# Optimization experiments

Hardware: AMD Instinct MI355X
Metric: run time of the kernel (lower is better)

Reference implementation:

```python
import jax, jax.numpy as jnp
import numpy as np

WINDOW_SIZE = 11
SIGMA = 1.5
C1 = (0.01 * 1.0) ** 2
C2 = (0.03 * 1.0) ** 2


def _gauss1d(k, sigma):
    x = np.arange(k, dtype=np.float64) - k // 2
    g = np.exp(-(x ** 2) / (2.0 * sigma ** 2)) / (np.sqrt(2.0 * np.pi) * sigma)
    return (g / g.sum()).astype(np.float32)


def _blur3d(x, g):
    # Separable 3D Gaussian blur, SAME padding. Math-equal to the full 11^3
    # kernel conv in the torch code since the 3D window is an outer product
    # of the normalized 1D Gaussian (symmetric, so conv == cross-corr).
    k = g.shape[0]
    p = k // 2
    dn = ('NCDHW', 'OIDHW', 'NCDHW')
    for axis in range(3):
        shape = [1, 1, 1, 1, 1]
        shape[2 + axis] = k
        w = jnp.asarray(g).reshape(shape)
        pad = [(0, 0), (0, 0), (0, 0)]
        pad[axis] = (p, p)
        x = jax.lax.conv_general_dilated(x, w, (1, 1, 1), pad, dimension_numbers=dn)
    return x


def setup_inputs() -> dict:
    key = jax.random.key(0)
    k1, k2 = jax.random.split(key)
    shape = (4, 1, 192, 192, 192)
    gt = jax.random.uniform(k1, shape, dtype=jnp.float32)
    pred = jax.random.uniform(k2, shape, dtype=jnp.float32)
    return {"gt": gt, "pred": pred}


def reference(gt, pred):
    g = _gauss1d(WINDOW_SIZE, SIGMA)
    mux = _blur3d(gt, g)
    muy = _blur3d(pred, g)
    mux_sq = mux * mux
    muy_sq = muy * muy
    mux_muy = mux * muy
    sigmax_sq = _blur3d(gt * gt, g) - mux_sq
    sigmay_sq = _blur3d(pred * pred, g) - muy_sq
    sigmaxy = _blur3d(gt * pred, g) - mux_muy
    ssim_map = ((2.0 * mux_muy + C1) * (2.0 * sigmaxy + C2)) / (
        (mux_sq + muy_sq + C1) * (sigmax_sq + sigmay_sq + C2))
    return jnp.mean(1.0 - ssim_map)
```

## Files before the change

### kernel.cpp

```cpp
#include <hip/hip_runtime.h>
#include <hip/hip_fp16.h>
#include <math.h>

namespace {
constexpr int S = 192;
constexpr long long S2 = (long long)S * S;
constexpr long long S3 = (long long)S * S2;
constexpr int NB = 4;
constexpr int K = 11;
constexpr int R = 5;
constexpr int HCH = 32;
constexpr int DCH = 48;
constexpr float C1f = 1e-4f;
constexpr float C2f = 9e-4f;

struct GaussW { float g[K]; };

__global__ void k_init(double* acc) { *acc = 0.0; }

__global__ void k_final(const double* __restrict__ acc, float* __restrict__ out) {
  out[0] = (float)(acc[0] / (double)(NB * S3));
}


template <int NROWS, bool GUARD>
__device__ __forceinline__ void stageA(const float* pg, const float* pp, int r0,
                                       int w, float2 (*rb)[208]) {
  float la[NROWS], lb[NROWS];
#pragma unroll
  for (int j = 0; j < NROWS; ++j) {
    int r = r0 + j;
    bool ok = !GUARD || ((unsigned)r < (unsigned)S);
    la[j] = ok ? pg[(long long)r * S + w] : 0.f;
    lb[j] = ok ? pp[(long long)r * S + w] : 0.f;
  }
#pragma unroll
  for (int j = 0; j < NROWS; ++j) rb[j][8 + w] = make_float2(la[j], lb[j]);
}

template <int NROWS, bool EMITALL>
__device__ __forceinline__ void consumeA(
    const float2 (*rb)[208], int w, const GaussW& Wt,
    float2 (&w01)[K], float2 (&w23)[K], float (&w4v)[K],
    uint2* p0123, __half* p4, long long obase, int hbase) {
#pragma unroll
  for (int j = 0; j < NROWS; ++j) {
    float2 s01 = make_float2(0.f, 0.f), s23 = make_float2(0.f, 0.f);
    float s4 = 0.f;
#pragma unroll
    for (int i = 0; i < K; ++i) {
      float2 ab = rb[j][w + 3 + i];
      float g = Wt.g[i];
      s01.x = fmaf(g, ab.x, s01.x);
      s01.y = fmaf(g, ab.y, s01.y);
      float ta = g * ab.x, tb = g * ab.y;
      s23.x = fmaf(ta, ab.x, s23.x);
      s23.y = fmaf(tb, ab.y, s23.y);
      s4 = fmaf(ta, ab.y, s4);
    }
    w01[j] = s01; w23[j] = s23; w4v[j] = s4;
    if (EMITALL || j == K - 1) {
      float2 m01 = make_float2(0.f, 0.f), m23 = make_float2(0.f, 0.f);
      float m4 = 0.f;
#pragma unroll
      for (int i = 0; i < K; ++i) {
        const int sl = (j + 1 + i) % K;
        float g = Wt.g[i];
        m01.x = fmaf(g, w01[sl].x, m01.x);
        m01.y = fmaf(g, w01[sl].y, m01.y);
        m23.x = fmaf(g, w23[sl].x, m23.x);
        m23.y = fmaf(g, w23[sl].y, m23.y);
        m4 = fmaf(g, w4v[sl], m4);
      }
      long long o = obase + (long long)(hbase + j) * S;
      __half2 h01 = __floats2half2_rn(m01.x, m01.y);
      __half2 h23 = __floats2half2_rn(m23.x, m23.y);
      uint2 v;
      v.x = __builtin_bit_cast(unsigned, h01);
      v.y = __builtin_bit_cast(unsigned, h23);
      p0123[o] = v;
      p4[o] = __float2half(m4);
    }
  }
}

__global__ __launch_bounds__(192) void k_blurWH(
    const float* __restrict__ gt, const float* __restrict__ pr,
    uint2* __restrict__ p0123, __half* __restrict__ p4,
    long long in_base, GaussW Wt) {
  __shared__ float2 rowbuf[K][208];
  const int w = threadIdx.x;
  const int dz = blockIdx.x;
  const int h0 = (int)blockIdx.y * HCH;
  const long long n = blockIdx.z;
  const float* pg = gt + in_base + (n * S + dz) * S2;
  const float* pp = pr + in_base + (n * S + dz) * S2;
  const long long obase = (n * S + dz) * S2 + w;

  if (w < 176) {
    int j = w >> 4, q = w & 15;
    rowbuf[j][(q < 8) ? q : (192 + q)] = make_float2(0.f, 0.f);
  }

  float2 w01[K], w23[K];
  float w4v[K];

  stageA<K, true>(pg, pp, h0 - R, w, rowbuf);
  __syncthreads();
  consumeA<K, false>(rowbuf, w, Wt, w01, w23, w4v, p0123, p4, obase, h0 - 10);
  __syncthreads();
  stageA<K, false>(pg, pp, h0 + 6, w, rowbuf);
  __syncthreads();
  consumeA<K, true>(rowbuf, w, Wt, w01, w23, w4v, p0123, p4, obase, h0 + 1);
  __syncthreads();
  stageA<K, false>(pg, pp, h0 + 17, w, rowbuf);
  __syncthreads();
  consumeA<K, true>(rowbuf, w, Wt, w01, w23, w4v, p0123, p4, obase, h0 + 12);
  __syncthreads();
  stageA<9, true>(pg, pp, h0 + 28, w, rowbuf);
  __syncthreads();
  consumeA<9, true>(rowbuf, w, Wt, w01, w23, w4v, p0123, p4, obase, h0 + 23);
}


template <int N, bool GUARD>
__device__ __forceinline__ void stageB(const uint2* q0123, const __half* q4,
                                       int plane0, uint2 (&sab)[K], __half (&se)[K]) {
#pragma unroll
  for (int j = 0; j < N; ++j) {
    int d = plane0 + j;
    bool ok = !GUARD || ((unsigned)d < (unsigned)S);
    long long o = (long long)d * S2;
    sab[j] = ok ? q0123[o] : make_uint2(0u, 0u);
    se[j] = ok ? q4[o] : __float2half(0.f);
  }
}

template <int NOUT>
__device__ __forceinline__ void consumeB(
    const uint2 (&sab)[K], const __half (&se)[K],
    const GaussW& Wt, float2 (&r01)[K], float2 (&r23)[K], float (&r4)[K],
    double& lsum) {
  float fsum = 0.f;
#pragma unroll
  for (int j = 0; j < NOUT; ++j) {
    const int sw = (10 + j) % K;
    r01[sw] = __half22float2(__builtin_bit_cast(__half2, sab[j].x));
    r23[sw] = __half22float2(__builtin_bit_cast(__half2, sab[j].y));
    r4[sw] = __half2float(se[j]);
    float2 m01 = make_float2(0.f, 0.f), m23 = make_float2(0.f, 0.f);
    float m4 = 0.f;
#pragma unroll
    for (int i = 0; i < K; ++i) {
      const int sl = (j + i) % K;
      float g = Wt.g[i];
      m01.x = fmaf(g, r01[sl].x, m01.x);
      m01.y = fmaf(g, r01[sl].y, m01.y);
      m23.x = fmaf(g, r23[sl].x, m23.x);
      m23.y = fmaf(g, r23[sl].y, m23.y);
      m4 = fmaf(g, r4[sl], m4);
    }
    float mux = m01.x, muy = m01.y, bxx = m23.x, byy = m23.y, bxy = m4;
    float mux2 = mux * mux, muy2 = muy * muy, muxy = mux * muy;
    float sx = bxx - mux2, sy = byy - muy2, sxy = bxy - muxy;
    float num = fmaf(2.f, muxy, C1f) * fmaf(2.f, sxy, C2f);
    float den = (mux2 + muy2 + C1f) * (sx + sy + C2f);
    fsum += 1.f - num * __builtin_amdgcn_rcpf(den);
  }
  lsum += (double)fsum;
}

__global__ __launch_bounds__(192) void k_blurD_ssim(
    const uint2* __restrict__ p0123, const __half* __restrict__ p4,
    double* __restrict__ acc, GaussW Wt) {
  const int w = threadIdx.x;
  const int h = blockIdx.x;
  const long long n = blockIdx.y;
  const int d0 = (int)blockIdx.z * DCH;
  const long long base = n * S3 + (long long)h * S + w;
  const uint2* q0123 = p0123 + base;
  const __half* q4 = p4 + base;

  float2 r01[K], r23[K];
  float r4[K];
#pragma unroll
  for (int c = 0; c < K - 1; ++c) {
    int d = d0 - R + c;
    if ((unsigned)d < (unsigned)S) {
      long long o = (long long)d * S2;
      uint2 v = q0123[o];
      r01[c] = __half22float2(__builtin_bit_cast(__half2, v.x));
      r23[c] = __half22float2(__builtin_bit_cast(__half2, v.y));
      r4[c] = __half2float(q4[o]);
    } else {
      r01[c] = make_float2(0.f, 0.f);
      r23[c] = make_float2(0.f, 0.f);
      r4[c] = 0.f;
    }
  }
  r01[K - 1] = make_float2(0.f, 0.f);
  r23[K - 1] = make_float2(0.f, 0.f);
  r4[K - 1] = 0.f;

  uint2 sab0[K], sab1[K];
  __half se0[K], se1[K];
  double lsum = 0.0;

  stageB<K, false>(q0123, q4, d0 + 5, sab0, se0);
  stageB<K, false>(q0123, q4, d0 + 16, sab1, se1);
  consumeB<K>(sab0, se0, Wt, r01, r23, r4, lsum);
  stageB<K, false>(q0123, q4, d0 + 27, sab0, se0);
  consumeB<K>(sab1, se1, Wt, r01, r23, r4, lsum);
  stageB<K, true>(q0123, q4, d0 + 38, sab1, se1);
  consumeB<K>(sab0, se0, Wt, r01, r23, r4, lsum);
  stageB<4, true>(q0123, q4, d0 + 49, sab0, se0);
  consumeB<K>(sab1, se1, Wt, r01, r23, r4, lsum);
  consumeB<4>(sab0, se0, Wt, r01, r23, r4, lsum);

  double v = lsum;
#pragma unroll
  for (int o = 32; o > 0; o >>= 1) v += __shfl_down(v, o, 64);
  __shared__ double wsum[3];
  int lane = threadIdx.x & 63, wv = threadIdx.x >> 6;
  if (lane == 0) wsum[wv] = v;
  __syncthreads();
  if (threadIdx.x == 0) atomicAdd(acc, wsum[0] + wsum[1] + wsum[2]);
}

}

extern "C" void kernel_launch(void* const* d_in, const int* in_sizes, int n_in,
                              void* d_out, int out_size, void* d_ws, size_t ws_size,
                              hipStream_t stream) {
  (void)in_sizes; (void)n_in; (void)out_size;
  const float* gt = (const float*)d_in[0];
  const float* pr = (const float*)d_in[1];
  float* out = (float*)d_out;
  double* acc = (double*)d_ws;

  GaussW W;
  {
    double gg[K], sum = 0.0;
    for (int i = 0; i < K; ++i) {
      double x = (double)(i - K / 2);
      gg[i] = exp(-(x * x) / (2.0 * 1.5 * 1.5)) / (sqrt(2.0 * M_PI) * 1.5);
      sum += gg[i];
    }
    for (int i = 0; i < K; ++i) W.g[i] = (float)(gg[i] / sum);
  }

  auto run = [&](long long base_n, int nb) {
    size_t vox = (size_t)nb * S3;
    uint2* p0123 = (uint2*)((char*)d_ws + 256);
    __half* p4 = (__half*)(p0123 + vox);
    k_blurWH<<<dim3(S, S / HCH, nb), dim3(192), 0, stream>>>(
        gt, pr, p0123, p4, base_n * S3, W);
    k_blurD_ssim<<<dim3(S, nb, S / DCH), dim3(192), 0, stream>>>(
        p0123, p4, acc, W);
  };
  auto need = [](int nb) { return (size_t)256 + (size_t)nb * S3 * 10; };

  k_init<<<dim3(1), dim3(1), 0, stream>>>(acc);
  if (ws_size >= need(2)) {
    run(0, 2);
    run(2, 2);
  } else {
    for (int g = 0; g < NB; ++g) run(g, 1);
  }
  k_final<<<dim3(1), dim3(1), 0, stream>>>(acc, out);
}
```

Baseline: 426.2 us.

## Give each wavefront its own LDS row tile and fold accumulator init into blur

The H/W blur kernel now splits its 192 threads into three 64-lane wavefronts. Each wavefront loads its own 64-column tile plus a 10-column halo into a private shared-memory slice, so every __syncthreads between the staging and consuming phases is removed. The separate accumulator-zeroing kernel is dropped, and one thread of the first blur launch clears the accumulator instead, saving a launch. The cost is some redundant halo loads and reliance on lockstep execution within a wave64 for LDS ordering, since no barrier separates the writes from the reads.

```diff
diff --git a/kernel.cpp b/kernel.cpp
--- a/kernel.cpp
+++ b/kernel.cpp
@@ -16,8 +16,6 @@
 
 struct GaussW { float g[K]; };
 
-__global__ void k_init(double* acc) { *acc = 0.0; }
-
 __global__ void k_final(const double* __restrict__ acc, float* __restrict__ out) {
   out[0] = (float)(acc[0] / (double)(NB * S3));
 }
@@ -25,22 +23,29 @@
 
 template <int NROWS, bool GUARD>
 __device__ __forceinline__ void stageA(const float* pg, const float* pp, int r0,
-                                       int w, float2 (*rb)[208]) {
-  float la[NROWS], lb[NROWS];
+                                       int l, int c1, bool c1ok, int c2, bool c2ok,
+                                       float2 (*rb)[76]) {
+  float a1[NROWS], b1[NROWS], a2[NROWS], b2[NROWS];
 #pragma unroll
   for (int j = 0; j < NROWS; ++j) {
     int r = r0 + j;
-    bool ok = !GUARD || ((unsigned)r < (unsigned)S);
-    la[j] = ok ? pg[(long long)r * S + w] : 0.f;
-    lb[j] = ok ? pp[(long long)r * S + w] : 0.f;
-  }
-#pragma unroll
-  for (int j = 0; j < NROWS; ++j) rb[j][8 + w] = make_float2(la[j], lb[j]);
+    bool rok = !GUARD || ((unsigned)r < (unsigned)S);
+    long long ro = (long long)r * S;
+    a1[j] = (rok && c1ok) ? pg[ro + c1] : 0.f;
+    b1[j] = (rok && c1ok) ? pp[ro + c1] : 0.f;
+    a2[j] = (rok && c2ok) ? pg[ro + c2] : 0.f;
+    b2[j] = (rok && c2ok) ? pp[ro + c2] : 0.f;
+  }
+#pragma unroll
+  for (int j = 0; j < NROWS; ++j) {
+    rb[j][l] = make_float2(a1[j], b1[j]);
+    if (l < 10) rb[j][64 + l] = make_float2(a2[j], b2[j]);
+  }
 }
 
 template <int NROWS, bool EMITALL>
 __device__ __forceinline__ void consumeA(
-    const float2 (*rb)[208], int w, const GaussW& Wt,
+    const float2 (*rb)[76], int l, const GaussW& Wt,
     float2 (&w01)[K], float2 (&w23)[K], float (&w4v)[K],
     uint2* p0123, __half* p4, long long obase, int hbase) {
 #pragma unroll
@@ -49,7 +54,7 @@
     float s4 = 0.f;
 #pragma unroll
     for (int i = 0; i < K; ++i) {
-      float2 ab = rb[j][w + 3 + i];
+      float2 ab = rb[j][l + i];
       float g = Wt.g[i];
       s01.x = fmaf(g, ab.x, s01.x);
       s01.y = fmaf(g, ab.y, s01.y);
@@ -87,39 +92,38 @@
 __global__ __launch_bounds__(192) void k_blurWH(
     const float* __restrict__ gt, const float* __restrict__ pr,
     uint2* __restrict__ p0123, __half* __restrict__ p4,
-    long long in_base, GaussW Wt) {
-  __shared__ float2 rowbuf[K][208];
+    long long in_base, GaussW Wt, double* __restrict__ acc, int zero_acc) {
+  __shared__ float2 rowbuf[3][K][76];
   const int w = threadIdx.x;
+  const int l = w & 63;
+  const int v = w >> 6;
   const int dz = blockIdx.x;
   const int h0 = (int)blockIdx.y * HCH;
   const long long n = blockIdx.z;
+
+  if (zero_acc && dz == 0 && blockIdx.y == 0 && n == 0 && w == 0) *acc = 0.0;
+
   const float* pg = gt + in_base + (n * S + dz) * S2;
   const float* pp = pr + in_base + (n * S + dz) * S2;
   const long long obase = (n * S + dz) * S2 + w;
 
-  if (w < 176) {
-    int j = w >> 4, q = w & 15;
-    rowbuf[j][(q < 8) ? q : (192 + q)] = make_float2(0.f, 0.f);
-  }
+  const int c1 = (v << 6) - 5 + l;
+  const bool c1ok = (unsigned)c1 < (unsigned)S;
+  const int c2 = (v << 6) + 59 + l;
+  const bool c2ok = (l < 10) && (c2 < S);
+  float2 (*rb)[76] = rowbuf[v];
 
   float2 w01[K], w23[K];
   float w4v[K];
 
-  stageA<K, true>(pg, pp, h0 - R, w, rowbuf);
-  __syncthreads();
-  consumeA<K, false>(rowbuf, w, Wt, w01, w23, w4v, p0123, p4, obase, h0 - 10);
-  __syncthreads();
-  stageA<K, false>(pg, pp, h0 + 6, w, rowbuf);
-  __syncthreads();
-  consumeA<K, true>(rowbuf, w, Wt, w01, w23, w4v, p0123, p4, obase, h0 + 1);
-  __syncthreads();
-  stageA<K, false>(pg, pp, h0 + 17, w, rowbuf);
-  __syncthreads();
-  consumeA<K, true>(rowbuf, w, Wt, w01, w23, w4v, p0123, p4, obase, h0 + 12);
-  __syncthreads();
-  stageA<9, true>(pg, pp, h0 + 28, w, rowbuf);
-  __syncthreads();
-  consumeA<9, true>(rowbuf, w, Wt, w01, w23, w4v, p0123, p4, obase, h0 + 23);
+  stageA<K, true>(pg, pp, h0 - R, l, c1, c1ok, c2, c2ok, rb);
+  consumeA<K, false>(rb, l, Wt, w01, w23, w4v, p0123, p4, obase, h0 - 10);
+  stageA<K, false>(pg, pp, h0 + 6, l, c1, c1ok, c2, c2ok, rb);
+  consumeA<K, true>(rb, l, Wt, w01, w23, w4v, p0123, p4, obase, h0 + 1);
+  stageA<K, false>(pg, pp, h0 + 17, l, c1, c1ok, c2, c2ok, rb);
+  consumeA<K, true>(rb, l, Wt, w01, w23, w4v, p0123, p4, obase, h0 + 12);
+  stageA<9, true>(pg, pp, h0 + 28, l, c1, c1ok, c2, c2ok, rb);
+  consumeA<9, true>(rb, l, Wt, w01, w23, w4v, p0123, p4, obase, h0 + 23);
 }
 
 
@@ -249,23 +253,22 @@
     for (int i = 0; i < K; ++i) W.g[i] = (float)(gg[i] / sum);
   }
 
-  auto run = [&](long long base_n, int nb) {
+  auto run = [&](long long base_n, int nb, int zero) {
     size_t vox = (size_t)nb * S3;
     uint2* p0123 = (uint2*)((char*)d_ws + 256);
     __half* p4 = (__half*)(p0123 + vox);
     k_blurWH<<<dim3(S, S / HCH, nb), dim3(192), 0, stream>>>(
-        gt, pr, p0123, p4, base_n * S3, W);
+        gt, pr, p0123, p4, base_n * S3, W, acc, zero);
     k_blurD_ssim<<<dim3(S, nb, S / DCH), dim3(192), 0, stream>>>(
         p0123, p4, acc, W);
   };
   auto need = [](int nb) { return (size_t)256 + (size_t)nb * S3 * 10; };
 
-  k_init<<<dim3(1), dim3(1), 0, stream>>>(acc);
   if (ws_size >= need(2)) {
-    run(0, 2);
-    run(2, 2);
+    run(0, 2, 1);
+    run(2, 2, 0);
   } else {
-    for (int g = 0; g < NB; ++g) run(g, 1);
+    for (int g = 0; g < NB; ++g) run(g, 1, g == 0);
   }
   k_final<<<dim3(1), dim3(1), 0, stream>>>(acc, out);
 }
```

Result: slower. 468.8 us (+10.0%).

## Double-buffer WH blur rows via async global_load_lds and shrink D chunk

Applied to the files above, without the earlier changes.

The WH blur kernel now splits its LDS into two buffers with separate gt/pred arrays. It uses global_load_lds 16-byte async copies to prefetch the next 11-row block while the current one is consumed, which drops one barrier per stage and hides load latency. The D-blur kernel cuts its depth chunk from 48 to 16 planes, tripling the grid size. That buys more parallelism and fewer registers per thread, at the cost of re-reading more halo planes. The LDS footprint doubles.

```diff
diff --git a/kernel.cpp b/kernel.cpp
--- a/kernel.cpp
+++ b/kernel.cpp
@@ -10,7 +10,8 @@
 constexpr int K = 11;
 constexpr int R = 5;
 constexpr int HCH = 32;
-constexpr int DCH = 48;
+constexpr int DCH = 16;
+constexpr int AROW = 208;
 constexpr float C1f = 1e-4f;
 constexpr float C2f = 9e-4f;
 
@@ -23,24 +24,36 @@
 }
 
 
+__device__ __forceinline__ void gll16(const float* gsrc, float* ldst) {
+  __builtin_amdgcn_global_load_lds(
+      (const __attribute__((address_space(1))) void*)gsrc,
+      (__attribute__((address_space(3))) void*)ldst, 16, 0, 0);
+}
+
 template <int NROWS, bool GUARD>
-__device__ __forceinline__ void stageA(const float* pg, const float* pp, int r0,
-                                       int w, float2 (*rb)[208]) {
-  float la[NROWS], lb[NROWS];
-#pragma unroll
-  for (int j = 0; j < NROWS; ++j) {
-    int r = r0 + j;
-    bool ok = !GUARD || ((unsigned)r < (unsigned)S);
-    la[j] = ok ? pg[(long long)r * S + w] : 0.f;
-    lb[j] = ok ? pp[(long long)r * S + w] : 0.f;
-  }
-#pragma unroll
-  for (int j = 0; j < NROWS; ++j) rb[j][8 + w] = make_float2(la[j], lb[j]);
+__device__ __forceinline__ void issueA(const float* pg, const float* pp,
+                                       int r0, int l, int v,
+                                       float (*buf)[K][AROW]) {
+#pragma unroll
+  for (int k = 0; k < (2 * NROWS + 2) / 3; ++k) {
+    int u = v + 3 * k;
+    if (u < 2 * NROWS) {
+      int row = u >> 1, arr = u & 1;
+      int r = r0 + row;
+      float* dst = &buf[arr][row][8];
+      if (!GUARD || (unsigned)r < (unsigned)S) {
+        const float* src = (arr ? pp : pg) + (long long)r * S + (l << 2);
+        if (l < 48) gll16(src, dst);
+      } else {
+        if (l < 48) *(float4*)(dst + (l << 2)) = make_float4(0.f, 0.f, 0.f, 0.f);
+      }
+    }
+  }
 }
 
 template <int NROWS, bool EMITALL>
 __device__ __forceinline__ void consumeA(
-    const float2 (*rb)[208], int w, const GaussW& Wt,
+    const float (*LA)[AROW], const float (*LB)[AROW], int w, const GaussW& Wt,
     float2 (&w01)[K], float2 (&w23)[K], float (&w4v)[K],
     uint2* p0123, __half* p4, long long obase, int hbase) {
 #pragma unroll
@@ -49,14 +62,15 @@
     float s4 = 0.f;
 #pragma unroll
     for (int i = 0; i < K; ++i) {
-      float2 ab = rb[j][w + 3 + i];
+      float a = LA[j][w + 3 + i];
+      float b = LB[j][w + 3 + i];
       float g = Wt.g[i];
-      s01.x = fmaf(g, ab.x, s01.x);
-      s01.y = fmaf(g, ab.y, s01.y);
-      float ta = g * ab.x, tb = g * ab.y;
-      s23.x = fmaf(ta, ab.x, s23.x);
-      s23.y = fmaf(tb, ab.y, s23.y);
-      s4 = fmaf(ta, ab.y, s4);
+      s01.x = fmaf(g, a, s01.x);
+      s01.y = fmaf(g, b, s01.y);
+      float ta = g * a, tb = g * b;
+      s23.x = fmaf(ta, a, s23.x);
+      s23.y = fmaf(tb, b, s23.y);
+      s4 = fmaf(ta, b, s4);
     }
     w01[j] = s01; w23[j] = s23; w4v[j] = s4;
     if (EMITALL || j == K - 1) {
@@ -88,8 +102,10 @@
     const float* __restrict__ gt, const float* __restrict__ pr,
     uint2* __restrict__ p0123, __half* __restrict__ p4,
     long long in_base, GaussW Wt) {
-  __shared__ float2 rowbuf[K][208];
+  __shared__ float lds[2][2][K][AROW];
   const int w = threadIdx.x;
+  const int l = w & 63;
+  const int v = w >> 6;
   const int dz = blockIdx.x;
   const int h0 = (int)blockIdx.y * HCH;
   const long long n = blockIdx.z;
@@ -97,35 +113,37 @@
   const float* pp = pr + in_base + (n * S + dz) * S2;
   const long long obase = (n * S + dz) * S2 + w;
 
-  if (w < 176) {
-    int j = w >> 4, q = w & 15;
-    rowbuf[j][(q < 8) ? q : (192 + q)] = make_float2(0.f, 0.f);
+  for (int q = w; q < 704; q += 192) {
+    int prw = q >> 4, p = q & 15;
+    int idx = (p < 8) ? p : (192 + p);
+    (&lds[0][0][0][0])[prw * AROW + idx] = 0.f;
   }
 
   float2 w01[K], w23[K];
   float w4v[K];
 
-  stageA<K, true>(pg, pp, h0 - R, w, rowbuf);
-  __syncthreads();
-  consumeA<K, false>(rowbuf, w, Wt, w01, w23, w4v, p0123, p4, obase, h0 - 10);
-  __syncthreads();
-  stageA<K, false>(pg, pp, h0 + 6, w, rowbuf);
-  __syncthreads();
-  consumeA<K, true>(rowbuf, w, Wt, w01, w23, w4v, p0123, p4, obase, h0 + 1);
-  __syncthreads();
-  stageA<K, false>(pg, pp, h0 + 17, w, rowbuf);
-  __syncthreads();
-  consumeA<K, true>(rowbuf, w, Wt, w01, w23, w4v, p0123, p4, obase, h0 + 12);
-  __syncthreads();
-  stageA<9, true>(pg, pp, h0 + 28, w, rowbuf);
-  __syncthreads();
-  consumeA<9, true>(rowbuf, w, Wt, w01, w23, w4v, p0123, p4, obase, h0 + 23);
+  issueA<K, true>(pg, pp, h0 - R, l, v, lds[0]);
+  __syncthreads();
+  issueA<K, false>(pg, pp, h0 + 6, l, v, lds[1]);
+  consumeA<K, false>(lds[0][0], lds[0][1], w, Wt, w01, w23, w4v,
+                     p0123, p4, obase, h0 - 10);
+  __syncthreads();
+  issueA<K, false>(pg, pp, h0 + 17, l, v, lds[0]);
+  consumeA<K, true>(lds[1][0], lds[1][1], w, Wt, w01, w23, w4v,
+                    p0123, p4, obase, h0 + 1);
+  __syncthreads();
+  issueA<9, true>(pg, pp, h0 + 28, l, v, lds[1]);
+  consumeA<K, true>(lds[0][0], lds[0][1], w, Wt, w01, w23, w4v,
+                    p0123, p4, obase, h0 + 12);
+  __syncthreads();
+  consumeA<9, true>(lds[1][0], lds[1][1], w, Wt, w01, w23, w4v,
+                    p0123, p4, obase, h0 + 23);
 }
 
 
 template <int N, bool GUARD>
 __device__ __forceinline__ void stageB(const uint2* q0123, const __half* q4,
-                                       int plane0, uint2 (&sab)[K], __half (&se)[K]) {
+                                       int plane0, uint2 (&sab)[N], __half (&se)[N]) {
 #pragma unroll
   for (int j = 0; j < N; ++j) {
     int d = plane0 + j;
@@ -138,7 +156,7 @@
 
 template <int NOUT>
 __device__ __forceinline__ void consumeB(
-    const uint2 (&sab)[K], const __half (&se)[K],
+    const uint2 (&sab)[NOUT], const __half (&se)[NOUT],
     const GaussW& Wt, float2 (&r01)[K], float2 (&r23)[K], float (&r4)[K],
     double& lsum) {
   float fsum = 0.f;
@@ -188,9 +206,9 @@
     int d = d0 - R + c;
     if ((unsigned)d < (unsigned)S) {
       long long o = (long long)d * S2;
-      uint2 v = q0123[o];
-      r01[c] = __half22float2(__builtin_bit_cast(__half2, v.x));
-      r23[c] = __half22float2(__builtin_bit_cast(__half2, v.y));
+      uint2 vv = q0123[o];
+      r01[c] = __half22float2(__builtin_bit_cast(__half2, vv.x));
+      r23[c] = __half22float2(__builtin_bit_cast(__half2, vv.y));
       r4[c] = __half2float(q4[o]);
     } else {
       r01[c] = make_float2(0.f, 0.f);
@@ -202,27 +220,21 @@
   r23[K - 1] = make_float2(0.f, 0.f);
   r4[K - 1] = 0.f;
 
-  uint2 sab0[K], sab1[K];
-  __half se0[K], se1[K];
+  uint2 sab0[K], sab1[5];
+  __half se0[K], se1[5];
   double lsum = 0.0;
 
   stageB<K, false>(q0123, q4, d0 + 5, sab0, se0);
-  stageB<K, false>(q0123, q4, d0 + 16, sab1, se1);
+  stageB<5, true>(q0123, q4, d0 + 16, sab1, se1);
   consumeB<K>(sab0, se0, Wt, r01, r23, r4, lsum);
-  stageB<K, false>(q0123, q4, d0 + 27, sab0, se0);
-  consumeB<K>(sab1, se1, Wt, r01, r23, r4, lsum);
-  stageB<K, true>(q0123, q4, d0 + 38, sab1, se1);
-  consumeB<K>(sab0, se0, Wt, r01, r23, r4, lsum);
-  stageB<4, true>(q0123, q4, d0 + 49, sab0, se0);
-  consumeB<K>(sab1, se1, Wt, r01, r23, r4, lsum);
-  consumeB<4>(sab0, se0, Wt, r01, r23, r4, lsum);
-
-  double v = lsum;
-#pragma unroll
-  for (int o = 32; o > 0; o >>= 1) v += __shfl_down(v, o, 64);
+  consumeB<5>(sab1, se1, Wt, r01, r23, r4, lsum);
+
+  double vv = lsum;
+#pragma unroll
+  for (int o = 32; o > 0; o >>= 1) vv += __shfl_down(vv, o, 64);
   __shared__ double wsum[3];
   int lane = threadIdx.x & 63, wv = threadIdx.x >> 6;
-  if (lane == 0) wsum[wv] = v;
+  if (lane == 0) wsum[wv] = vv;
   __syncthreads();
   if (threadIdx.x == 0) atomicAdd(acc, wsum[0] + wsum[1] + wsum[2]);
 }
```

Measured after the change: 499.1 us. 17.1% more time.

## Software-pipeline batches by fusing D-blur of previous volume with WH-blur of next

Applied to the files above, without the earlier changes.

Splits both kernel bodies into device functions and adds a mixed kernel whose blocks either run the depth-blur+SSIM on the previous volume or the W/H blur on the next volume, using double-buffered intermediates. The point is to overlap the compute-heavy and memory-heavy phases and reduce the tail and launch gaps between them. The trade-off is per-volume launches of smaller grids instead of two-volume batches, plus the added branch divergence and the shared-memory footprint of the larger branch in every block.

```diff
diff --git a/kernel.cpp b/kernel.cpp
--- a/kernel.cpp
+++ b/kernel.cpp
@@ -84,18 +84,14 @@
   }
 }
 
-__global__ __launch_bounds__(192) void k_blurWH(
+__device__ __forceinline__ void bodyA(
     const float* __restrict__ gt, const float* __restrict__ pr,
     uint2* __restrict__ p0123, __half* __restrict__ p4,
-    long long in_base, GaussW Wt) {
-  __shared__ float2 rowbuf[K][208];
-  const int w = threadIdx.x;
-  const int dz = blockIdx.x;
-  const int h0 = (int)blockIdx.y * HCH;
-  const long long n = blockIdx.z;
-  const float* pg = gt + in_base + (n * S + dz) * S2;
-  const float* pp = pr + in_base + (n * S + dz) * S2;
-  const long long obase = (n * S + dz) * S2 + w;
+    long long in_base, const GaussW& Wt, int dz, int h0, int w,
+    float2 (*rowbuf)[208]) {
+  const float* pg = gt + in_base + (long long)dz * S2;
+  const float* pp = pr + in_base + (long long)dz * S2;
+  const long long obase = (long long)dz * S2 + w;
 
   if (w < 176) {
     int j = w >> 4, q = w & 15;
@@ -170,14 +166,11 @@
   lsum += (double)fsum;
 }
 
-__global__ __launch_bounds__(192) void k_blurD_ssim(
+__device__ __forceinline__ void bodyB(
     const uint2* __restrict__ p0123, const __half* __restrict__ p4,
-    double* __restrict__ acc, GaussW Wt) {
-  const int w = threadIdx.x;
-  const int h = blockIdx.x;
-  const long long n = blockIdx.y;
-  const int d0 = (int)blockIdx.z * DCH;
-  const long long base = n * S3 + (long long)h * S + w;
+    double* __restrict__ acc, const GaussW& Wt, int h, int d0, int w,
+    double* wsum ) {
+  const long long base = (long long)h * S + w;
   const uint2* q0123 = p0123 + base;
   const __half* q4 = p4 + base;
 
@@ -220,11 +213,46 @@
   double v = lsum;
 #pragma unroll
   for (int o = 32; o > 0; o >>= 1) v += __shfl_down(v, o, 64);
+  int lane = w & 63, wv = w >> 6;
+  if (lane == 0) wsum[wv] = v;
+  __syncthreads();
+  if (w == 0) atomicAdd(acc, wsum[0] + wsum[1] + wsum[2]);
+}
+
+
+__global__ __launch_bounds__(192) void k_blurWH(
+    const float* __restrict__ gt, const float* __restrict__ pr,
+    uint2* __restrict__ p0123, __half* __restrict__ p4,
+    long long in_base, GaussW Wt) {
+  __shared__ float2 rowbuf[K][208];
+  bodyA(gt, pr, p0123, p4, in_base, Wt, (int)blockIdx.x,
+        (int)blockIdx.y * HCH, (int)threadIdx.x, rowbuf);
+}
+
+__global__ __launch_bounds__(192) void k_blurD_ssim(
+    const uint2* __restrict__ p0123, const __half* __restrict__ p4,
+    double* __restrict__ acc, GaussW Wt) {
   __shared__ double wsum[3];
-  int lane = threadIdx.x & 63, wv = threadIdx.x >> 6;
-  if (lane == 0) wsum[wv] = v;
-  __syncthreads();
-  if (threadIdx.x == 0) atomicAdd(acc, wsum[0] + wsum[1] + wsum[2]);
+  bodyB(p0123, p4, acc, Wt, (int)blockIdx.x, (int)blockIdx.y * DCH,
+        (int)threadIdx.x, wsum);
+}
+
+__global__ __launch_bounds__(192) void k_mixed(
+    const float* __restrict__ gt, const float* __restrict__ pr,
+    uint2* __restrict__ pA0123, __half* __restrict__ pA4, long long inA_base,
+    const uint2* __restrict__ pB0123, const __half* __restrict__ pB4,
+    double* __restrict__ acc, GaussW Wt, int nB) {
+  __shared__ float2 rowbuf[K][208];
+  const int bid = (int)blockIdx.x;
+  const int w = (int)threadIdx.x;
+  if (bid < nB) {
+    int h = bid % S, dc = bid / S;
+    bodyB(pB0123, pB4, acc, Wt, h, dc * DCH, w, (double*)rowbuf);
+  } else {
+    int b = bid - nB;
+    int dz = b % S, hc = b / S;
+    bodyA(gt, pr, pA0123, pA4, inA_base, Wt, dz, hc * HCH, w, rowbuf);
+  }
 }
 
 }
@@ -249,23 +277,39 @@
     for (int i = 0; i < K; ++i) W.g[i] = (float)(gg[i] / sum);
   }
 
-  auto run = [&](long long base_n, int nb) {
-    size_t vox = (size_t)nb * S3;
-    uint2* p0123 = (uint2*)((char*)d_ws + 256);
-    __half* p4 = (__half*)(p0123 + vox);
-    k_blurWH<<<dim3(S, S / HCH, nb), dim3(192), 0, stream>>>(
-        gt, pr, p0123, p4, base_n * S3, W);
-    k_blurD_ssim<<<dim3(S, nb, S / DCH), dim3(192), 0, stream>>>(
-        p0123, p4, acc, W);
-  };
-  auto need = [](int nb) { return (size_t)256 + (size_t)nb * S3 * 10; };
+  const size_t bufBytes = (size_t)S3 * 10;
+  const size_t need2 = 256 + 2 * bufBytes;
+  const size_t need1 = 256 + bufBytes;
+  char* wsb = (char*)d_ws + 256;
+  uint2* p0[2];
+  __half* p4b[2];
+  p0[0] = (uint2*)wsb;
+  p4b[0] = (__half*)(p0[0] + (size_t)S3);
+  p0[1] = (uint2*)(wsb + bufBytes);
+  p4b[1] = (__half*)(p0[1] + (size_t)S3);
+
+  const int nB = S * (S / DCH);
+  const int nA = S * (S / HCH);
 
   k_init<<<dim3(1), dim3(1), 0, stream>>>(acc);
-  if (ws_size >= need(2)) {
-    run(0, 2);
-    run(2, 2);
+  if (ws_size >= need2) {
+    k_blurWH<<<dim3(S, S / HCH), dim3(192), 0, stream>>>(
+        gt, pr, p0[0], p4b[0], 0, W);
+    for (int c = 1; c < NB; ++c) {
+      k_mixed<<<dim3(nB + nA), dim3(192), 0, stream>>>(
+          gt, pr, p0[c & 1], p4b[c & 1], (long long)c * S3,
+          p0[(c - 1) & 1], p4b[(c - 1) & 1], acc, W, nB);
+    }
+    k_blurD_ssim<<<dim3(S, S / DCH), dim3(192), 0, stream>>>(
+        p0[(NB - 1) & 1], p4b[(NB - 1) & 1], acc, W);
   } else {
-    for (int g = 0; g < NB; ++g) run(g, 1);
+    (void)need1;
+    for (int c = 0; c < NB; ++c) {
+      k_blurWH<<<dim3(S, S / HCH), dim3(192), 0, stream>>>(
+          gt, pr, p0[0], p4b[0], (long long)c * S3, W);
+      k_blurD_ssim<<<dim3(S, S / DCH), dim3(192), 0, stream>>>(
+          p0[0], p4b[0], acc, W);
+    }
   }
   k_final<<<dim3(1), dim3(1), 0, stream>>>(acc, out);
 }
```

Measured after the change: 493.2 us. 15.7% more time.
